# Kernel optimization log

Measured on AMD Instinct MI355X. Metric: run time of the kernel, lower is better.

Reference implementation:

```python
import jax, jax.numpy as jnp
import numpy as np

N = 100000   # num nodes
E = 1200000  # num edges
D = 64       # feature dim (input and both hidden layers)
R = 4        # num relations


def setup_inputs() -> dict:
    key = jax.random.key(0)
    ks = jax.random.split(key, 16)

    def p(k, shape, scale=0.05):
        return jax.random.normal(k, shape, dtype=jnp.float32) * scale

    inp = {
        "x": p(ks[0], (N, D), 1.0),
        "src": jax.random.randint(ks[1], (E,), 0, N),
        "dst": jax.random.randint(ks[2], (E,), 0, N),
        "rel": jax.random.randint(ks[3], (E,), 0, R),
    }
    i = 4
    for layer in (1, 2):
        inp[f"conv{layer}_w"] = p(ks[i], (D, R * D)); i += 1
        inp[f"conv{layer}_b"] = jnp.zeros((D,), jnp.float32)
        inp[f"conv{layer}_ws"] = p(ks[i], (D, D)); i += 1
        inp[f"conv{layer}_bs"] = jnp.zeros((D,), jnp.float32)
        inp[f"hw{layer}_pw"] = p(ks[i], (D, 2 * D)); i += 1
        inp[f"hw{layer}_pb"] = jnp.zeros((D,), jnp.float32)
        inp[f"hw{layer}_tw"] = p(ks[i], (D, 2 * D)); i += 1
        inp[f"hw{layer}_tb"] = jnp.full((D,), -2.0, jnp.float32)  # transform bias init -2
    return inp


def _rgc(x, src, dst, rel, w, b, ws, bs):
    # RelationalGraphConv: per-(node, relation) scatter-mean of source features,
    # then linear over concatenated relation slots + self-loop linear + sigmoid.
    msg = x[src]                                  # [E, D] gather
    seg = dst * R + rel                           # [E] flattened (node, relation) id
    s = jax.ops.segment_sum(msg, seg, num_segments=N * R)          # [N*R, D]
    cnt = jax.ops.segment_sum(jnp.ones((msg.shape[0], 1), msg.dtype), seg,
                              num_segments=N * R)                  # [N*R, 1]
    upd = (s / jnp.maximum(cnt, 1.0)).reshape(N, R * x.shape[1])   # [N, R*D]
    out = upd @ w.T + b + x @ ws.T + bs
    return jax.nn.sigmoid(out)


def _highway(h, prev, pw, pb, tw, tb):
    c = jnp.concatenate([h, prev], axis=1)        # [N, 2D]
    pr = jax.nn.relu(c @ pw.T + pb)
    g = jax.nn.sigmoid(c @ tw.T + tb)
    return g * pr + (1.0 - g) * h


def reference(x, src, dst, rel,
              conv1_w, conv1_b, conv1_ws, conv1_bs,
              hw1_pw, hw1_pb, hw1_tw, hw1_tb,
              conv2_w, conv2_b, conv2_ws, conv2_bs,
              hw2_pw, hw2_pb, hw2_tw, hw2_tb):
    h1 = _rgc(x, src, dst, rel, conv1_w, conv1_b, conv1_ws, conv1_bs)
    g1 = _highway(h1, x, hw1_pw, hw1_pb, hw1_tw, hw1_tb)   # prev_gcn = input
    h2 = _rgc(g1, src, dst, rel, conv2_w, conv2_b, conv2_ws, conv2_bs)
    g2 = _highway(h2, h1, hw2_pw, hw2_pb, hw2_tw, hw2_tb)  # prev_gcn = h1 (conv1 output)
    return g2  # node_feature, [N, D]
```

## Files before the change

kernel.cpp:

```cpp
#include <hip/hip_runtime.h>

#define NN 100000
#define NE 1200000
#define NRR 400000
#define NBIN 98
#define EPB 4096

typedef float f32x4 __attribute__((ext_vector_type(4)));
typedef __bf16 bf16x8 __attribute__((ext_vector_type(8)));

__device__ __forceinline__ float sigmoidf_(float x){ return 1.0f/(1.0f+__expf(-x)); }

__global__ __launch_bounds__(256)
void binhist_kernel(const int* __restrict__ dst, const int* __restrict__ rel,
                    int* __restrict__ bincnt){
  __shared__ int h[NBIN];
  int t = threadIdx.x;
  if (t < NBIN) h[t] = 0;
  __syncthreads();
  for (int e = blockIdx.x*256 + t; e < NE; e += 512*256){
    int bin = (dst[e]*4 + rel[e]) >> 12;
    atomicAdd(&h[bin], 1);
  }
  __syncthreads();
  if (t < NBIN && h[t]) atomicAdd(&bincnt[t], h[t]);
}

__global__ void binscan_kernel(const int* __restrict__ bincnt, int* __restrict__ binoff,
                               int* __restrict__ bincur, int* __restrict__ soff){
  if (threadIdx.x == 0){
    int s = 0;
    for (int i = 0; i < NBIN; ++i){ binoff[i] = s; bincur[i] = s; s += bincnt[i]; }
    binoff[NBIN] = NE;
    soff[NRR] = NE;
  }
}

__global__ __launch_bounds__(256)
void passA_kernel(const int* __restrict__ src, const int* __restrict__ dst,
                  const int* __restrict__ rel, int* __restrict__ bincur,
                  unsigned* __restrict__ ebin){
  __shared__ int h[NBIN], runbase[NBIN];
  int t = threadIdx.x;
  if (t < NBIN) h[t] = 0;
  __syncthreads();
  int lo = blockIdx.x*EPB, hi = min(lo + EPB, NE);
  for (int e = lo + t; e < hi; e += 256)
    atomicAdd(&h[(dst[e]*4 + rel[e]) >> 12], 1);
  __syncthreads();
  if (t < NBIN){
    runbase[t] = h[t] ? atomicAdd(&bincur[t], h[t]) : 0;
    h[t] = 0;
  }
  __syncthreads();
  for (int e = lo + t; e < hi; e += 256){
    int seg = dst[e]*4 + rel[e];
    int bin = seg >> 12;
    int p = runbase[bin] + atomicAdd(&h[bin], 1);
    ebin[p] = (unsigned)src[e] | ((unsigned)(seg & 4095) << 17);
  }
}

__global__ __launch_bounds__(1024)
void passB_kernel(const unsigned* __restrict__ ebin, const int* __restrict__ binoff,
                  int* __restrict__ soff, unsigned* __restrict__ ebuck){
  __shared__ int st[4096];
  __shared__ int wsum[16], wbase[16];
  const int bin = blockIdx.x;
  const int t = threadIdx.x;
  const int base = binoff[bin], end = binoff[bin+1];
  #pragma unroll
  for (int i = 0; i < 4; ++i) st[t*4 + i] = 0;
  __syncthreads();
  for (int e = base + t; e < end; e += 1024)
    atomicAdd(&st[(ebin[e] >> 17) & 4095], 1);
  __syncthreads();
  int h0 = st[t*4], h1 = st[t*4+1], h2 = st[t*4+2], h3 = st[t*4+3];
  int lsum = h0 + h1 + h2 + h3;
  int lane = t & 63, wv = t >> 6;
  int inc = lsum;
  #pragma unroll
  for (int o = 1; o < 64; o <<= 1){ int u = __shfl_up(inc, o); if (lane >= o) inc += u; }
  if (lane == 63) wsum[wv] = inc;
  __syncthreads();
  if (t == 0){ int s = 0; for (int i = 0; i < 16; ++i){ wbase[i] = s; s += wsum[i]; } }
  __syncthreads();
  int ex = base + wbase[wv] + (inc - lsum);
  int s0 = ex, s1 = ex + h0, s2 = s1 + h1, s3 = s2 + h2;
  st[t*4] = s0; st[t*4+1] = s1; st[t*4+2] = s2; st[t*4+3] = s3;
  int sg = bin*4096 + t*4;
  if (sg   < NRR) soff[sg]   = s0;
  if (sg+1 < NRR) soff[sg+1] = s1;
  if (sg+2 < NRR) soff[sg+2] = s2;
  if (sg+3 < NRR) soff[sg+3] = s3;
  __syncthreads();
  for (int e = base + t; e < end; e += 1024){
    unsigned u = ebin[e];
    int p = atomicAdd(&st[(u >> 17) & 4095], 1);
    ebuck[p] = u & 0x1FFFFu;
  }
}

__global__ void tobf16_kernel(const float* __restrict__ xf, __bf16* __restrict__ xb){
  int i = (blockIdx.x*256 + threadIdx.x)*8;
  if (i < NN*64){
    f32x4 a = *(const f32x4*)(xf + i);
    f32x4 b = *(const f32x4*)(xf + i + 4);
    bf16x8 r;
    r[0]=(__bf16)a[0]; r[1]=(__bf16)a[1]; r[2]=(__bf16)a[2]; r[3]=(__bf16)a[3];
    r[4]=(__bf16)b[0]; r[5]=(__bf16)b[1]; r[6]=(__bf16)b[2]; r[7]=(__bf16)b[3];
    *(bf16x8*)(xb + i) = r;
  }
}

__global__ void prep_kernel(const float* __restrict__ w,  const float* __restrict__ b,
                            const float* __restrict__ ws, const float* __restrict__ bs,
                            const float* __restrict__ pw, const float* __restrict__ pb,
                            const float* __restrict__ tw, const float* __restrict__ tb,
                            const float* __restrict__ w2,  const float* __restrict__ b2,
                            const float* __restrict__ ws2, const float* __restrict__ bs2,
                            const float* __restrict__ pw2, const float* __restrict__ pb2,
                            const float* __restrict__ tw2, const float* __restrict__ tb2,
                            __bf16* __restrict__ W1a, __bf16* __restrict__ W2a,
                            float* __restrict__ B1a, float* __restrict__ B2a,
                            __bf16* __restrict__ W1b, __bf16* __restrict__ W2b,
                            float* __restrict__ B1b, float* __restrict__ B2b){
  int i = blockIdx.x*256 + threadIdx.x;
  if (i < 64*320) {
    int e = i & 7, lane = (i >> 3) & 63, j = (i >> 9) & 3, kbi = i >> 11;
    int n = j*16 + (lane & 15);
    int k = kbi*32 + (lane >> 4)*8 + e;
    float va = (k < 256) ? w[n*256 + k]  : ws[n*64 + (k - 256)];
    float vb = (k < 256) ? w2[n*256 + k] : ws2[n*64 + (k - 256)];
    W1a[i] = (__bf16)va;
    W1b[i] = (__bf16)vb;
  }
  if (i < 128*128) {
    int e = i & 7, lane = (i >> 3) & 63, j = (i >> 9) & 7, kbi = i >> 12;
    int n = j*16 + (lane & 15);
    int k = kbi*32 + (lane >> 4)*8 + e;
    float va = (n < 64) ? pw[n*128 + k]  : tw[(n - 64)*128 + k];
    float vb = (n < 64) ? pw2[n*128 + k] : tw2[(n - 64)*128 + k];
    W2a[i] = (__bf16)va;
    W2b[i] = (__bf16)vb;
  }
  if (i < 64)  { B1a[i] = b[i] + bs[i];  B1b[i] = b2[i] + bs2[i]; }
  if (i < 128) { B2a[i] = (i < 64) ? pb[i] : tb[i-64];
                 B2b[i] = (i < 64) ? pb2[i] : tb2[i-64]; }
}

__global__ __launch_bounds__(256)
void gather_kernel(const unsigned* __restrict__ ebuck, const int* __restrict__ soff,
                   const __bf16* __restrict__ inb, __bf16* __restrict__ segb){
  const int sgg = blockIdx.x*32 + (threadIdx.x >> 3);
  const int fl  = threadIdx.x & 7;
  const int e0 = soff[sgg];
  const int e1 = soff[sgg + 1];
  const int c  = e1 - e0;

  f32x4 a0 = {0.f,0.f,0.f,0.f}, a1 = {0.f,0.f,0.f,0.f};
  f32x4 b0 = {0.f,0.f,0.f,0.f}, b1 = {0.f,0.f,0.f,0.f};
  int i = 0;
  for (; i + 2 <= c; i += 2){
    int s0 = (int)ebuck[e0 + i];
    int s1 = (int)ebuck[e0 + i + 1];
    bf16x8 v0 = *(const bf16x8*)(&inb[(size_t)s0*64 + fl*8]);
    bf16x8 v1 = *(const bf16x8*)(&inb[(size_t)s1*64 + fl*8]);
    a0[0]+=(float)v0[0]; a0[1]+=(float)v0[1]; a0[2]+=(float)v0[2]; a0[3]+=(float)v0[3];
    a1[0]+=(float)v0[4]; a1[1]+=(float)v0[5]; a1[2]+=(float)v0[6]; a1[3]+=(float)v0[7];
    b0[0]+=(float)v1[0]; b0[1]+=(float)v1[1]; b0[2]+=(float)v1[2]; b0[3]+=(float)v1[3];
    b1[0]+=(float)v1[4]; b1[1]+=(float)v1[5]; b1[2]+=(float)v1[6]; b1[3]+=(float)v1[7];
  }
  if (i < c){
    int s0 = (int)ebuck[e0 + i];
    bf16x8 v0 = *(const bf16x8*)(&inb[(size_t)s0*64 + fl*8]);
    a0[0]+=(float)v0[0]; a0[1]+=(float)v0[1]; a0[2]+=(float)v0[2]; a0[3]+=(float)v0[3];
    a1[0]+=(float)v0[4]; a1[1]+=(float)v0[5]; a1[2]+=(float)v0[6]; a1[3]+=(float)v0[7];
  }
  float inv = 1.0f / fmaxf((float)c, 1.0f);
  bf16x8 r;
  r[0]=(__bf16)((a0[0]+b0[0])*inv); r[1]=(__bf16)((a0[1]+b0[1])*inv);
  r[2]=(__bf16)((a0[2]+b0[2])*inv); r[3]=(__bf16)((a0[3]+b0[3])*inv);
  r[4]=(__bf16)((a1[0]+b1[0])*inv); r[5]=(__bf16)((a1[1]+b1[1])*inv);
  r[6]=(__bf16)((a1[2]+b1[2])*inv); r[7]=(__bf16)((a1[3]+b1[3])*inv);

  const int n   = sgg >> 2, rr = sgg & 3;
  const int nb  = n >> 4,  ml = n & 15;
  const int kbi = rr*2 + (fl >> 2);
  const int kgs = fl & 3;
  *(bf16x8*)(&segb[(size_t)((nb*8 + kbi)*64 + kgs*16 + ml)*8]) = r;
}

#define HSP 72

template<bool LAYER1>
__global__ __launch_bounds__(256, 4)
void dense_kernel(const __bf16* __restrict__ segbs,
                  const __bf16* __restrict__ xinb,
                  const __bf16* __restrict__ prevb,
                  const __bf16* __restrict__ W1s,
                  const __bf16* __restrict__ W2s,
                  const float* __restrict__ bias1,
                  const float* __restrict__ bias2,
                  __bf16* __restrict__ hb,
                  __bf16* __restrict__ gb,
                  float* __restrict__ outp)
{
  __shared__ __align__(16) __bf16 hs[64*HSP];
  __shared__ __align__(16) float outs[64*64];

  const int tid  = threadIdx.x;
  const int lane = tid & 63;
  const int wv   = tid >> 6;
  const int mloc = lane & 15;
  const int kg   = lane >> 4;
  const int wb   = blockIdx.x*64 + wv*16;
  const int arow = min(wb + mloc, NN-1);
  const int nbq  = min(wb, NN-16) >> 4;
  const size_t abase = (size_t)nbq * (8*512);

  f32x4 acc1[4] = {};

  #pragma unroll
  for (int kbi = 0; kbi < 8; ++kbi) {
    bf16x8 af = *(const bf16x8*)(&segbs[abase + (size_t)(kbi*64 + lane)*8]);
    #pragma unroll
    for (int j = 0; j < 4; ++j) {
      bf16x8 bf = *(const bf16x8*)(&W1s[((kbi*4 + j)*64 + lane)*8]);
      acc1[j] = __builtin_amdgcn_mfma_f32_16x16x32_bf16(af, bf, acc1[j], 0,0,0);
    }
  }
  #pragma unroll
  for (int kb = 0; kb < 64; kb += 32) {
    bf16x8 af = *(const bf16x8*)(&xinb[(size_t)arow*64 + kb + kg*8]);
    const int kbi = 8 + (kb >> 5);
    #pragma unroll
    for (int j = 0; j < 4; ++j) {
      bf16x8 bf = *(const bf16x8*)(&W1s[((kbi*4 + j)*64 + lane)*8]);
      acc1[j] = __builtin_amdgcn_mfma_f32_16x16x32_bf16(af, bf, acc1[j], 0,0,0);
    }
  }

  #pragma unroll
  for (int j = 0; j < 4; ++j) {
    int col = j*16 + mloc;
    float b1 = bias1[col];
    #pragma unroll
    for (int r = 0; r < 4; ++r) {
      float hv = sigmoidf_(acc1[j][r] + b1);
      acc1[j][r] = hv;
      hs[(wv*16 + kg*4 + r)*HSP + col] = (__bf16)hv;
    }
  }

  if (LAYER1) {
    #pragma unroll
    for (int i = 0; i < 2; ++i) {
      int r2 = i*8 + (lane >> 3);
      int c2 = lane & 7;
      bf16x8 v = *(const bf16x8*)(&hs[(wv*16 + r2)*HSP + c2*8]);
      int grow = wb + r2;
      if (grow < NN) *(bf16x8*)(&hb[(size_t)grow*64 + c2*8]) = v;
    }
  }

  f32x4 acc2[8] = {};
  #pragma unroll
  for (int kb = 0; kb < 64; kb += 32) {
    bf16x8 af = *(const bf16x8*)(&hs[(wv*16 + mloc)*HSP + kb + kg*8]);
    const int kbi = kb >> 5;
    #pragma unroll
    for (int j = 0; j < 8; ++j) {
      bf16x8 bf = *(const bf16x8*)(&W2s[((kbi*8 + j)*64 + lane)*8]);
      acc2[j] = __builtin_amdgcn_mfma_f32_16x16x32_bf16(af, bf, acc2[j], 0,0,0);
    }
  }
  #pragma unroll
  for (int kb = 0; kb < 64; kb += 32) {
    bf16x8 af = *(const bf16x8*)(&prevb[(size_t)arow*64 + kb + kg*8]);
    const int kbi = 2 + (kb >> 5);
    #pragma unroll
    for (int j = 0; j < 8; ++j) {
      bf16x8 bf = *(const bf16x8*)(&W2s[((kbi*8 + j)*64 + lane)*8]);
      acc2[j] = __builtin_amdgcn_mfma_f32_16x16x32_bf16(af, bf, acc2[j], 0,0,0);
    }
  }

  #pragma unroll
  for (int j = 0; j < 4; ++j) {
    int col = j*16 + mloc;
    float bp = bias2[col];
    float bt = bias2[64 + col];
    #pragma unroll
    for (int r = 0; r < 4; ++r) {
      float pr = fmaxf(acc2[j][r] + bp, 0.0f);
      float g  = sigmoidf_(acc2[j+4][r] + bt);
      float hv = acc1[j][r];
      float ov = g*pr + (1.0f - g)*hv;
      if (LAYER1) {
        hs[(wv*16 + kg*4 + r)*HSP + col] = (__bf16)ov;
      } else {
        outs[(wv*16 + kg*4 + r)*64 + col] = ov;
      }
    }
  }
  if (LAYER1) {
    #pragma unroll
    for (int i = 0; i < 2; ++i) {
      int r2 = i*8 + (lane >> 3);
      int c2 = lane & 7;
      bf16x8 v = *(const bf16x8*)(&hs[(wv*16 + r2)*HSP + c2*8]);
      int grow = wb + r2;
      if (grow < NN) *(bf16x8*)(&gb[(size_t)grow*64 + c2*8]) = v;
    }
  } else {
    #pragma unroll
    for (int i = 0; i < 4; ++i) {
      int pos = i*256 + lane*4;
      int r2 = pos >> 6, c2 = pos & 63;
      int grow = wb + r2;
      if (grow < NN)
        *(f32x4*)(&outp[(size_t)grow*64 + c2]) =
            *(const f32x4*)(&outs[(wv*16 + r2)*64 + c2]);
    }
  }
}

extern "C" void kernel_launch(void* const* d_in, const int* in_sizes, int n_in,
                              void* d_out, int out_size, void* d_ws, size_t ws_size,
                              hipStream_t stream){
  const float* x    = (const float*)d_in[0];
  const int*   src  = (const int*)d_in[1];
  const int*   dst  = (const int*)d_in[2];
  const int*   rel  = (const int*)d_in[3];
  const float* c1w  = (const float*)d_in[4];
  const float* c1b  = (const float*)d_in[5];
  const float* c1ws = (const float*)d_in[6];
  const float* c1bs = (const float*)d_in[7];
  const float* h1pw = (const float*)d_in[8];
  const float* h1pb = (const float*)d_in[9];
  const float* h1tw = (const float*)d_in[10];
  const float* h1tb = (const float*)d_in[11];
  const float* c2w  = (const float*)d_in[12];
  const float* c2b  = (const float*)d_in[13];
  const float* c2ws = (const float*)d_in[14];
  const float* c2bs = (const float*)d_in[15];
  const float* h2pw = (const float*)d_in[16];
  const float* h2pb = (const float*)d_in[17];
  const float* h2tw = (const float*)d_in[18];
  const float* h2tb = (const float*)d_in[19];

  char* p = (char*)d_ws;
  __bf16* segb = (__bf16*)p;  p += (size_t)NRR*64*2;
  __bf16* xb   = (__bf16*)p;  p += (size_t)NN*64*2;
  __bf16* h1b  = (__bf16*)p;  p += (size_t)NN*64*2;
  __bf16* g1b  = (__bf16*)p;  p += (size_t)NN*64*2;
  unsigned* ebuck = (unsigned*)p; p += (size_t)NE*4;
  unsigned* ebin  = (unsigned*)p; p += (size_t)NE*4;
  int* soff    = (int*)p;     p += (size_t)(NRR+8)*4;
  int* bincnt  = (int*)p;     p += 128*4;
  int* binoff  = (int*)p;     p += 128*4;
  int* bincur  = (int*)p;     p += 128*4;
  __bf16* W1a  = (__bf16*)p;  p += 64*320*2;
  __bf16* W2a  = (__bf16*)p;  p += 128*128*2;
  __bf16* W1b  = (__bf16*)p;  p += 64*320*2;
  __bf16* W2b  = (__bf16*)p;  p += 128*128*2;
  float* B1a   = (float*)p;   p += 64*4;
  float* B2a   = (float*)p;   p += 128*4;
  float* B1b   = (float*)p;   p += 64*4;
  float* B2b   = (float*)p;   p += 128*4;

  float* out = (float*)d_out;

  hipMemsetAsync(bincnt, 0, 128*4, stream);
  binhist_kernel<<<512, 256, 0, stream>>>(dst, rel, bincnt);
  binscan_kernel<<<1, 64, 0, stream>>>(bincnt, binoff, bincur, soff);
  passA_kernel<<<(NE+EPB-1)/EPB, 256, 0, stream>>>(src, dst, rel, bincur, ebin);
  passB_kernel<<<NBIN, 1024, 0, stream>>>(ebin, binoff, soff, ebuck);

  tobf16_kernel<<<(NN*64/8 + 255)/256, 256, 0, stream>>>(x, xb);
  prep_kernel<<<80, 256, 0, stream>>>(c1w, c1b, c1ws, c1bs, h1pw, h1pb, h1tw, h1tb,
                                      c2w, c2b, c2ws, c2bs, h2pw, h2pb, h2tw, h2tb,
                                      W1a, W2a, B1a, B2a, W1b, W2b, B1b, B2b);

  gather_kernel<<<NRR/32, 256, 0, stream>>>(ebuck, soff, xb, segb);
  dense_kernel<true><<<(NN+63)/64, 256, 0, stream>>>(segb, xb, xb, W1a, W2a, B1a, B2a,
                                                     h1b, g1b, nullptr);
  gather_kernel<<<NRR/32, 256, 0, stream>>>(ebuck, soff, g1b, segb);
  dense_kernel<false><<<(NN+63)/64, 256, 0, stream>>>(segb, g1b, h1b, W1b, W2b, B1b, B2b,
                                                      nullptr, nullptr, out);
}
```

Measured before the change: 298.4 us.

## Use finer sort bins, fuse bf16 conversion with weight prep, prefetch gather indices

The counting sort now uses 392 bins of 1024 segments instead of 98 bins of 4096, so passB runs four times as many blocks with one segment per thread and a smaller shared histogram. The x-to-bf16 conversion and the weight-packing kernel are merged into a single launch. The gather kernel loads the first eight edge indices up front and issues their row loads unrolled to expose more memory parallelism, padding ebuck so these reads stay in bounds. The trade-offs are more global bin atomics and a serial scan over more bins in binscan, plus speculative index loads past short segments.

```diff
diff --git a/kernel.cpp b/kernel.cpp
--- a/kernel.cpp
+++ b/kernel.cpp
@@ -3,7 +3,8 @@
 #define NN 100000
 #define NE 1200000
 #define NRR 400000
-#define NBIN 98
+#define NBIN 392
+#define SEGB 1024
 #define EPB 4096
 
 typedef float f32x4 __attribute__((ext_vector_type(4)));
@@ -16,14 +17,15 @@
                     int* __restrict__ bincnt){
   __shared__ int h[NBIN];
   int t = threadIdx.x;
-  if (t < NBIN) h[t] = 0;
+  for (int i = t; i < NBIN; i += 256) h[i] = 0;
   __syncthreads();
   for (int e = blockIdx.x*256 + t; e < NE; e += 512*256){
-    int bin = (dst[e]*4 + rel[e]) >> 12;
+    int bin = (dst[e]*4 + rel[e]) >> 10;
     atomicAdd(&h[bin], 1);
   }
   __syncthreads();
-  if (t < NBIN && h[t]) atomicAdd(&bincnt[t], h[t]);
+  for (int i = t; i < NBIN; i += 256)
+    if (h[i]) atomicAdd(&bincnt[i], h[i]);
 }
 
 __global__ void binscan_kernel(const int* __restrict__ bincnt, int* __restrict__ binoff,
@@ -42,90 +44,87 @@
                   unsigned* __restrict__ ebin){
   __shared__ int h[NBIN], runbase[NBIN];
   int t = threadIdx.x;
-  if (t < NBIN) h[t] = 0;
+  for (int i = t; i < NBIN; i += 256) h[i] = 0;
   __syncthreads();
   int lo = blockIdx.x*EPB, hi = min(lo + EPB, NE);
   for (int e = lo + t; e < hi; e += 256)
-    atomicAdd(&h[(dst[e]*4 + rel[e]) >> 12], 1);
-  __syncthreads();
-  if (t < NBIN){
-    runbase[t] = h[t] ? atomicAdd(&bincur[t], h[t]) : 0;
-    h[t] = 0;
+    atomicAdd(&h[(dst[e]*4 + rel[e]) >> 10], 1);
+  __syncthreads();
+  for (int i = t; i < NBIN; i += 256){
+    runbase[i] = h[i] ? atomicAdd(&bincur[i], h[i]) : 0;
+    h[i] = 0;
   }
   __syncthreads();
   for (int e = lo + t; e < hi; e += 256){
     int seg = dst[e]*4 + rel[e];
-    int bin = seg >> 12;
+    int bin = seg >> 10;
     int p = runbase[bin] + atomicAdd(&h[bin], 1);
-    ebin[p] = (unsigned)src[e] | ((unsigned)(seg & 4095) << 17);
+    ebin[p] = (unsigned)src[e] | ((unsigned)(seg & 1023) << 17);
   }
 }
 
 __global__ __launch_bounds__(1024)
 void passB_kernel(const unsigned* __restrict__ ebin, const int* __restrict__ binoff,
                   int* __restrict__ soff, unsigned* __restrict__ ebuck){
-  __shared__ int st[4096];
+  __shared__ int st[SEGB];
   __shared__ int wsum[16], wbase[16];
   const int bin = blockIdx.x;
   const int t = threadIdx.x;
   const int base = binoff[bin], end = binoff[bin+1];
-  #pragma unroll
-  for (int i = 0; i < 4; ++i) st[t*4 + i] = 0;
+  st[t] = 0;
   __syncthreads();
   for (int e = base + t; e < end; e += 1024)
-    atomicAdd(&st[(ebin[e] >> 17) & 4095], 1);
-  __syncthreads();
-  int h0 = st[t*4], h1 = st[t*4+1], h2 = st[t*4+2], h3 = st[t*4+3];
-  int lsum = h0 + h1 + h2 + h3;
+    atomicAdd(&st[(ebin[e] >> 17) & 1023], 1);
+  __syncthreads();
+  int h0 = st[t];
   int lane = t & 63, wv = t >> 6;
-  int inc = lsum;
+  int inc = h0;
   #pragma unroll
   for (int o = 1; o < 64; o <<= 1){ int u = __shfl_up(inc, o); if (lane >= o) inc += u; }
   if (lane == 63) wsum[wv] = inc;
   __syncthreads();
   if (t == 0){ int s = 0; for (int i = 0; i < 16; ++i){ wbase[i] = s; s += wsum[i]; } }
   __syncthreads();
-  int ex = base + wbase[wv] + (inc - lsum);
-  int s0 = ex, s1 = ex + h0, s2 = s1 + h1, s3 = s2 + h2;
-  st[t*4] = s0; st[t*4+1] = s1; st[t*4+2] = s2; st[t*4+3] = s3;
-  int sg = bin*4096 + t*4;
-  if (sg   < NRR) soff[sg]   = s0;
-  if (sg+1 < NRR) soff[sg+1] = s1;
-  if (sg+2 < NRR) soff[sg+2] = s2;
-  if (sg+3 < NRR) soff[sg+3] = s3;
+  int ex = base + wbase[wv] + (inc - h0);
+  st[t] = ex;
+  int sg = bin*SEGB + t;
+  if (sg < NRR) soff[sg] = ex;
   __syncthreads();
   for (int e = base + t; e < end; e += 1024){
     unsigned u = ebin[e];
-    int p = atomicAdd(&st[(u >> 17) & 4095], 1);
+    int p = atomicAdd(&st[(u >> 17) & 1023], 1);
     ebuck[p] = u & 0x1FFFFu;
   }
 }
 
-__global__ void tobf16_kernel(const float* __restrict__ xf, __bf16* __restrict__ xb){
-  int i = (blockIdx.x*256 + threadIdx.x)*8;
-  if (i < NN*64){
-    f32x4 a = *(const f32x4*)(xf + i);
-    f32x4 b = *(const f32x4*)(xf + i + 4);
-    bf16x8 r;
-    r[0]=(__bf16)a[0]; r[1]=(__bf16)a[1]; r[2]=(__bf16)a[2]; r[3]=(__bf16)a[3];
-    r[4]=(__bf16)b[0]; r[5]=(__bf16)b[1]; r[6]=(__bf16)b[2]; r[7]=(__bf16)b[3];
-    *(bf16x8*)(xb + i) = r;
-  }
-}
-
-__global__ void prep_kernel(const float* __restrict__ w,  const float* __restrict__ b,
-                            const float* __restrict__ ws, const float* __restrict__ bs,
-                            const float* __restrict__ pw, const float* __restrict__ pb,
-                            const float* __restrict__ tw, const float* __restrict__ tb,
-                            const float* __restrict__ w2,  const float* __restrict__ b2,
-                            const float* __restrict__ ws2, const float* __restrict__ bs2,
-                            const float* __restrict__ pw2, const float* __restrict__ pb2,
-                            const float* __restrict__ tw2, const float* __restrict__ tb2,
-                            __bf16* __restrict__ W1a, __bf16* __restrict__ W2a,
-                            float* __restrict__ B1a, float* __restrict__ B2a,
-                            __bf16* __restrict__ W1b, __bf16* __restrict__ W2b,
-                            float* __restrict__ B1b, float* __restrict__ B2b){
-  int i = blockIdx.x*256 + threadIdx.x;
+#define TBB 3125
+__global__ __launch_bounds__(256)
+void tobf16_prep_kernel(const float* __restrict__ xf, __bf16* __restrict__ xb,
+                        const float* __restrict__ w,  const float* __restrict__ b,
+                        const float* __restrict__ ws, const float* __restrict__ bs,
+                        const float* __restrict__ pw, const float* __restrict__ pb,
+                        const float* __restrict__ tw, const float* __restrict__ tb,
+                        const float* __restrict__ w2,  const float* __restrict__ b2,
+                        const float* __restrict__ ws2, const float* __restrict__ bs2,
+                        const float* __restrict__ pw2, const float* __restrict__ pb2,
+                        const float* __restrict__ tw2, const float* __restrict__ tb2,
+                        __bf16* __restrict__ W1a, __bf16* __restrict__ W2a,
+                        float* __restrict__ B1a, float* __restrict__ B2a,
+                        __bf16* __restrict__ W1b, __bf16* __restrict__ W2b,
+                        float* __restrict__ B1b, float* __restrict__ B2b){
+  if (blockIdx.x < TBB) {
+    int i = (blockIdx.x*256 + threadIdx.x)*8;
+    if (i < NN*64){
+      f32x4 a = *(const f32x4*)(xf + i);
+      f32x4 c = *(const f32x4*)(xf + i + 4);
+      bf16x8 r;
+      r[0]=(__bf16)a[0]; r[1]=(__bf16)a[1]; r[2]=(__bf16)a[2]; r[3]=(__bf16)a[3];
+      r[4]=(__bf16)c[0]; r[5]=(__bf16)c[1]; r[6]=(__bf16)c[2]; r[7]=(__bf16)c[3];
+      *(bf16x8*)(xb + i) = r;
+    }
+    return;
+  }
+  int i = (blockIdx.x - TBB)*256 + threadIdx.x;
   if (i < 64*320) {
     int e = i & 7, lane = (i >> 3) & 63, j = (i >> 9) & 3, kbi = i >> 11;
     int n = j*16 + (lane & 15);
@@ -158,24 +157,36 @@
   const int e1 = soff[sgg + 1];
   const int c  = e1 - e0;
 
+  int idx[8];
+  #pragma unroll
+  for (int k = 0; k < 8; ++k) idx[k] = (int)ebuck[e0 + k];
+
   f32x4 a0 = {0.f,0.f,0.f,0.f}, a1 = {0.f,0.f,0.f,0.f};
   f32x4 b0 = {0.f,0.f,0.f,0.f}, b1 = {0.f,0.f,0.f,0.f};
-  int i = 0;
-  for (; i + 2 <= c; i += 2){
-    int s0 = (int)ebuck[e0 + i];
-    int s1 = (int)ebuck[e0 + i + 1];
-    bf16x8 v0 = *(const bf16x8*)(&inb[(size_t)s0*64 + fl*8]);
-    bf16x8 v1 = *(const bf16x8*)(&inb[(size_t)s1*64 + fl*8]);
-    a0[0]+=(float)v0[0]; a0[1]+=(float)v0[1]; a0[2]+=(float)v0[2]; a0[3]+=(float)v0[3];
-    a1[0]+=(float)v0[4]; a1[1]+=(float)v0[5]; a1[2]+=(float)v0[6]; a1[3]+=(float)v0[7];
-    b0[0]+=(float)v1[0]; b0[1]+=(float)v1[1]; b0[2]+=(float)v1[2]; b0[3]+=(float)v1[3];
-    b1[0]+=(float)v1[4]; b1[1]+=(float)v1[5]; b1[2]+=(float)v1[6]; b1[3]+=(float)v1[7];
-  }
-  if (i < c){
+  #pragma unroll
+  for (int k = 0; k < 8; ++k) {
+    if (k < c) {
+      bf16x8 v = *(const bf16x8*)(&inb[(size_t)idx[k]*64 + fl*8]);
+      if (k & 1) {
+        b0[0]+=(float)v[0]; b0[1]+=(float)v[1]; b0[2]+=(float)v[2]; b0[3]+=(float)v[3];
+        b1[0]+=(float)v[4]; b1[1]+=(float)v[5]; b1[2]+=(float)v[6]; b1[3]+=(float)v[7];
+      } else {
+        a0[0]+=(float)v[0]; a0[1]+=(float)v[1]; a0[2]+=(float)v[2]; a0[3]+=(float)v[3];
+        a1[0]+=(float)v[4]; a1[1]+=(float)v[5]; a1[2]+=(float)v[6]; a1[3]+=(float)v[7];
+      }
+    }
+  }
+  for (int i = 8; i < c; i += 2) {
     int s0 = (int)ebuck[e0 + i];
     bf16x8 v0 = *(const bf16x8*)(&inb[(size_t)s0*64 + fl*8]);
     a0[0]+=(float)v0[0]; a0[1]+=(float)v0[1]; a0[2]+=(float)v0[2]; a0[3]+=(float)v0[3];
     a1[0]+=(float)v0[4]; a1[1]+=(float)v0[5]; a1[2]+=(float)v0[6]; a1[3]+=(float)v0[7];
+    if (i + 1 < c) {
+      int s1 = (int)ebuck[e0 + i + 1];
+      bf16x8 v1 = *(const bf16x8*)(&inb[(size_t)s1*64 + fl*8]);
+      b0[0]+=(float)v1[0]; b0[1]+=(float)v1[1]; b0[2]+=(float)v1[2]; b0[3]+=(float)v1[3];
+      b1[0]+=(float)v1[4]; b1[1]+=(float)v1[5]; b1[2]+=(float)v1[6]; b1[3]+=(float)v1[7];
+    }
   }
   float inv = 1.0f / fmaxf((float)c, 1.0f);
   bf16x8 r;
@@ -355,12 +366,12 @@
   __bf16* xb   = (__bf16*)p;  p += (size_t)NN*64*2;
   __bf16* h1b  = (__bf16*)p;  p += (size_t)NN*64*2;
   __bf16* g1b  = (__bf16*)p;  p += (size_t)NN*64*2;
-  unsigned* ebuck = (unsigned*)p; p += (size_t)NE*4;
+  unsigned* ebuck = (unsigned*)p; p += (size_t)(NE+16)*4;
   unsigned* ebin  = (unsigned*)p; p += (size_t)NE*4;
   int* soff    = (int*)p;     p += (size_t)(NRR+8)*4;
-  int* bincnt  = (int*)p;     p += 128*4;
-  int* binoff  = (int*)p;     p += 128*4;
-  int* bincur  = (int*)p;     p += 128*4;
+  int* bincnt  = (int*)p;     p += 512*4;
+  int* binoff  = (int*)p;     p += 512*4;
+  int* bincur  = (int*)p;     p += 512*4;
   __bf16* W1a  = (__bf16*)p;  p += 64*320*2;
   __bf16* W2a  = (__bf16*)p;  p += 128*128*2;
   __bf16* W1b  = (__bf16*)p;  p += 64*320*2;
@@ -372,14 +383,14 @@
 
   float* out = (float*)d_out;
 
-  hipMemsetAsync(bincnt, 0, 128*4, stream);
+  hipMemsetAsync(bincnt, 0, 512*4, stream);
   binhist_kernel<<<512, 256, 0, stream>>>(dst, rel, bincnt);
   binscan_kernel<<<1, 64, 0, stream>>>(bincnt, binoff, bincur, soff);
   passA_kernel<<<(NE+EPB-1)/EPB, 256, 0, stream>>>(src, dst, rel, bincur, ebin);
   passB_kernel<<<NBIN, 1024, 0, stream>>>(ebin, binoff, soff, ebuck);
 
-  tobf16_kernel<<<(NN*64/8 + 255)/256, 256, 0, stream>>>(x, xb);
-  prep_kernel<<<80, 256, 0, stream>>>(c1w, c1b, c1ws, c1bs, h1pw, h1pb, h1tw, h1tb,
+  tobf16_prep_kernel<<<TBB+80, 256, 0, stream>>>(x, xb,
+                                      c1w, c1b, c1ws, c1bs, h1pw, h1pb, h1tw, h1tb,
                                       c2w, c2b, c2ws, c2bs, h2pw, h2pb, h2tw, h2tb,
                                       W1a, W2a, B1a, B2a, W1b, W2b, B1b, B2b);
 
```

Result: no change. 300.4 us (+0.7%).
